# Kernel optimization log

Measured on AMD Instinct MI355X. Metric: run time of the kernel, lower is better.

Reference implementation:

```python
import jax, jax.numpy as jnp
import numpy as np

N = 50000      # nodes
E = 250000     # edges (pairs) per key
DIN = 256
DOUT = 256
OH = 16        # one_hot_length
T = 2          # params['t']


def setup_inputs() -> dict:
    key = jax.random.key(0)
    ks = jax.random.split(key, 16)
    s_in = 1.0 / np.float32(np.sqrt(DIN))
    s_tr = 1.0 / np.float32(np.sqrt(DIN + OH))
    return {
        "h": jax.random.normal(ks[0], (N, DIN), jnp.float32),
        "pairs_k0": jax.random.randint(ks[1], (T, E), 0, N),
        "pairs_k1": jax.random.randint(ks[2], (T, E), 0, N),
        "degrees_k0": jax.random.uniform(ks[3], (T, E, OH), jnp.float32),
        "degrees_k1": jax.random.uniform(ks[4], (T, E, OH), jnp.float32),
        "scatter_k0": jax.random.randint(ks[5], (E,), 0, N),
        "scatter_k1": jax.random.randint(ks[6], (E,), 0, N),
        "W_lin": jax.random.normal(ks[7], (DIN, DOUT), jnp.float32) * s_in,
        "b_lin": jax.random.normal(ks[8], (DOUT,), jnp.float32) * 0.01,
        "W_k0": jax.random.normal(ks[9], (DIN + OH, DOUT), jnp.float32) * s_tr,
        "b_k0": jax.random.normal(ks[10], (DOUT,), jnp.float32) * 0.01,
        "W_k1": jax.random.normal(ks[11], (DIN + OH, DOUT), jnp.float32) * s_tr,
        "b_k1": jax.random.normal(ks[12], (DOUT,), jnp.float32) * 0.01,
        "eps_k0": jnp.zeros((1,), jnp.float32),
        "eps_k1": jnp.zeros((1,), jnp.float32),
    }


def _key_term(h, pairs, degrees, W, b, scatter, eps):
    # combination == 'multi': product over t of sigmoid(Linear([h[pairs_i], deg_i]))
    h_temp = jnp.ones((pairs.shape[1], W.shape[1]), h.dtype)
    for i in range(T):
        h_t = jnp.concatenate([h[pairs[i]], degrees[i]], axis=1)  # [E, DIN+OH]
        h_temp = h_temp * jax.nn.sigmoid(h_t @ W + b)             # [E, DOUT]
    h_sum = jax.ops.segment_sum(h_temp, scatter, num_segments=N)  # [N, DOUT]
    return (1.0 + eps) * h_sum                                    # scalar eps (shape [1])


def reference(h, pairs_k0, pairs_k1, degrees_k0, degrees_k1,
              scatter_k0, scatter_k1, W_lin, b_lin,
              W_k0, b_k0, W_k1, b_k1, eps_k0, eps_k1):
    h3 = h @ W_lin + b_lin
    h3 = h3 + _key_term(h, pairs_k0, degrees_k0, W_k0, b_k0, scatter_k0, eps_k0)
    h3 = h3 + _key_term(h, pairs_k1, degrees_k1, W_k1, b_k1, scatter_k1, eps_k1)
    return h3
```

## Files before the change

kernel.cpp:

```cpp
#include <hip/hip_runtime.h>
#include <hip/hip_bf16.h>

#define N_NODES 50000
#define N_EDGES 250000
#define DIN_ 256
#define DOUT_ 256
#define OH_ 16
#define KF_ 288
#define NBLK_EDGE ((N_EDGES + 63) / 64)
#define NBLK_G ((N_NODES + 63) / 64)
#define SCAN_TOT (2 * N_NODES)
#define SCAN_NB ((SCAN_TOT + 255) / 256)
#define NB_CONV ((N_NODES * DIN_ / 8) / 256)
#define NB_PREP ((DOUT_ * KF_ + 255) / 256)
#define NB_HIST ((N_EDGES + 255) / 256)

typedef short short8 __attribute__((ext_vector_type(8)));
typedef float f32x4 __attribute__((ext_vector_type(4)));

__device__ __forceinline__ unsigned short f2bf(float f) {
    unsigned u = __builtin_bit_cast(unsigned, f);
    return (unsigned short)((u + 0x7fffu + ((u >> 16) & 1u)) >> 16);
}

__device__ __forceinline__ float bf2f(unsigned v) {
    return __builtin_bit_cast(float, v << 16);
}

__device__ __forceinline__ uint4 pack8(float f0, float f1, float f2, float f3,
                                       float f4, float f5, float f6, float f7) {
    uint4 u;
    u.x = (unsigned)f2bf(f0) | ((unsigned)f2bf(f1) << 16);
    u.y = (unsigned)f2bf(f2) | ((unsigned)f2bf(f3) << 16);
    u.z = (unsigned)f2bf(f4) | ((unsigned)f2bf(f5) << 16);
    u.w = (unsigned)f2bf(f6) | ((unsigned)f2bf(f7) << 16);
    return u;
}

__device__ __forceinline__ float fast_rcp(float x) {
#if __has_builtin(__builtin_amdgcn_rcpf)
    return __builtin_amdgcn_rcpf(x);
#else
    return 1.0f / x;
#endif
}

__device__ __forceinline__ void gl_lds16(const void* g, void* l) {
    __builtin_amdgcn_global_load_lds(
        (const __attribute__((address_space(1))) unsigned int*)g,
        (__attribute__((address_space(3))) unsigned int*)l, 16, 0, 0);
}

__global__ void fused_prep(const float* __restrict__ h, unsigned short* __restrict__ hbf,
                           const float* __restrict__ W_lin,
                           const float* __restrict__ W_k0,
                           const float* __restrict__ W_k1,
                           unsigned short* __restrict__ WT_lin,
                           unsigned short* __restrict__ WT_k0,
                           unsigned short* __restrict__ WT_k1,
                           const int* __restrict__ sc0, const int* __restrict__ sc1,
                           int* __restrict__ hist) {
    int bx = blockIdx.x;
    if (bx < NB_CONV) {
        int idx = bx * 256 + threadIdx.x;
        const f32x4* s = (const f32x4*)(h + (size_t)idx * 8);
        f32x4 a = s[0], b = s[1];
        ((uint4*)hbf)[idx] = pack8(a[0], a[1], a[2], a[3], b[0], b[1], b[2], b[3]);
    } else if (bx < NB_CONV + NB_PREP) {
        int idx = (bx - NB_CONV) * 256 + threadIdx.x;
        if (idx < DOUT_ * DIN_) {
            int n = idx >> 8, k = idx & 255;
            WT_lin[idx] = f2bf(W_lin[k * DOUT_ + n]);
        }
        if (idx < DOUT_ * KF_) {
            int n = idx / KF_, k = idx - n * KF_;
            float v0 = 0.f, v1 = 0.f;
            if (k < DIN_ + OH_) {
                v0 = W_k0[k * DOUT_ + n];
                v1 = W_k1[k * DOUT_ + n];
            }
            WT_k0[idx] = f2bf(v0);
            WT_k1[idx] = f2bf(v1);
        }
    } else {
        int e = (bx - NB_CONV - NB_PREP) * 256 + threadIdx.x;
        if (e < N_EDGES) {
            atomicAdd(&hist[sc0[e]], 1);
            atomicAdd(&hist[N_NODES + sc1[e]], 1);
        }
    }
}

__global__ void scan_pass1(const int* __restrict__ hist, int* __restrict__ partials) {
    __shared__ int sdata[256];
    int gid = blockIdx.x * 256 + threadIdx.x;
    sdata[threadIdx.x] = (gid < SCAN_TOT) ? hist[gid] : 0;
    __syncthreads();
    for (int d = 128; d > 0; d >>= 1) {
        if (threadIdx.x < d) sdata[threadIdx.x] += sdata[threadIdx.x + d];
        __syncthreads();
    }
    if (threadIdx.x == 0) partials[blockIdx.x] = sdata[0];
}

__global__ __launch_bounds__(512) void scan_pass2(int* __restrict__ partials) {
    __shared__ int s[512];
    int t = threadIdx.x;
    s[t] = (t < SCAN_NB) ? partials[t] : 0;
    __syncthreads();
    for (int d = 1; d < 512; d <<= 1) {
        int add = (t >= d) ? s[t - d] : 0;
        __syncthreads();
        s[t] += add;
        __syncthreads();
    }
    if (t < SCAN_NB) partials[t] = (t == 0) ? 0 : s[t - 1];
}

__global__ void scan_pass3(const int* __restrict__ hist, const int* __restrict__ partials,
                           int* __restrict__ offs) {
    __shared__ int s[256];
    int gid = blockIdx.x * 256 + threadIdx.x;
    int t = threadIdx.x;
    int v = (gid < SCAN_TOT) ? hist[gid] : 0;
    s[t] = v;
    __syncthreads();
    for (int d = 1; d < 256; d <<= 1) {
        int add = (t >= d) ? s[t - d] : 0;
        __syncthreads();
        s[t] += add;
        __syncthreads();
    }
    if (gid < SCAN_TOT) offs[gid] = partials[blockIdx.x] + s[t] - v;
}

__global__ __launch_bounds__(256) void rank_lin(const int* __restrict__ sc0,
                                                const int* __restrict__ sc1,
                                                int* __restrict__ offs,
                                                int* __restrict__ order,
                                                int* __restrict__ keys,
                                                const unsigned short* __restrict__ hbf,
                                                const unsigned short* __restrict__ WT_lin,
                                                const unsigned short* __restrict__ WTk0,
                                                const unsigned short* __restrict__ WTk1,
                                                const float* __restrict__ b_lin,
                                                const float* __restrict__ bk0,
                                                const float* __restrict__ bk1,
                                                float* __restrict__ out,
                                                unsigned short* __restrict__ G0,
                                                unsigned short* __restrict__ G1) {
    if (blockIdx.x >= 3 * NBLK_G) {
        int e = (blockIdx.x - 3 * NBLK_G) * 256 + threadIdx.x;
        if (e < N_EDGES) {
            int k0 = sc0[e];
            int p = atomicAdd(&offs[k0], 1);
            order[p] = e; keys[p] = k0;
            int k1 = sc1[e];
            int q = atomicAdd(&offs[N_NODES + k1], 1);
            order[q] = e; keys[q] = k1;
        }
        return;
    }
    __shared__ unsigned short Alds[2][64][32];
    __shared__ unsigned short Blds[2][256][32];
    __shared__ float bias_lds[256];
    int kb = blockIdx.x / NBLK_G;
    int bx = blockIdx.x - kb * NBLK_G;
    const unsigned short* WT; const float* bias; int stride;
    if (kb == 0)      { WT = WTk0;   bias = bk0;   stride = KF_; }
    else if (kb == 1) { WT = WTk1;   bias = bk1;   stride = KF_; }
    else              { WT = WT_lin; bias = b_lin; stride = DIN_; }

    int tid = threadIdx.x;
    int w = tid >> 6, ln = tid & 63, l15 = ln & 15;
    int row0 = bx * 64;
    bias_lds[tid] = bias[tid];

    int ar = row0 + w * 16 + (ln >> 2);
    if (ar >= N_NODES) ar = N_NODES - 1;
    int qs = (ln & 3) ^ ((ln >> 3) & 3);
    const unsigned short* asrc = hbf + (size_t)ar * DIN_ + qs * 8;
    int brow = w * 64;
    int swz = ((ln >> 4) ^ ((l15 >> 1) & 3)) * 8;

    f32x4 acc[16];
#pragma unroll
    for (int j = 0; j < 16; ++j) acc[j] = (f32x4)(0.f);

    gl_lds16(asrc, &Alds[0][w * 16][0]);
#pragma unroll
    for (int i = 0; i < 4; ++i) {
        int n = brow + i * 16 + (ln >> 2);
        gl_lds16(WT + (size_t)n * stride + qs * 8, &Blds[0][brow + i * 16][0]);
    }
    __syncthreads();

    int buf = 0;
    for (int kk = 0; kk < 8; ++kk) {
        if (kk < 7) {
            gl_lds16(asrc + (kk + 1) * 32, &Alds[buf ^ 1][w * 16][0]);
#pragma unroll
            for (int i = 0; i < 4; ++i) {
                int n = brow + i * 16 + (ln >> 2);
                gl_lds16(WT + (size_t)n * stride + (kk + 1) * 32 + qs * 8,
                         &Blds[buf ^ 1][brow + i * 16][0]);
            }
        }
        short8 af = *(const short8*)&Alds[buf][w * 16 + l15][swz];
#pragma unroll
        for (int j = 0; j < 16; ++j) {
            short8 bf = *(const short8*)&Blds[buf][j * 16 + l15][swz];
            acc[j] = __builtin_amdgcn_mfma_f32_16x16x32_bf16(af, bf, acc[j], 0, 0, 0);
        }
        __syncthreads();
        buf ^= 1;
    }

    int rbase = row0 + w * 16 + ((ln >> 4) << 2);
    unsigned short* G = (kb == 0) ? G0 : G1;
#pragma unroll
    for (int j = 0; j < 16; ++j) {
        int n = j * 16 + l15;
        float bv = bias_lds[n];
#pragma unroll
        for (int i = 0; i < 4; ++i) {
            int rr = rbase + i;
            if (rr < N_NODES) {
                float v = acc[j][i] + bv;
                if (kb == 2) out[(size_t)rr * DOUT_ + n] = v;
                else         G[(size_t)rr * DOUT_ + n] = f2bf(v);
            }
        }
    }
}

__global__ __launch_bounds__(256, 4) void edge_fused(const unsigned short* __restrict__ Gk0,
                                                     const unsigned short* __restrict__ Gk1,
                                                     const int* __restrict__ pairs0,
                                                     const int* __restrict__ pairs1,
                                                     const float* __restrict__ deg0,
                                                     const float* __restrict__ deg1,
                                                     const int* __restrict__ order_all,
                                                     const int* __restrict__ keys_all,
                                                     const unsigned short* __restrict__ WT0,
                                                     const unsigned short* __restrict__ WT1,
                                                     const float* __restrict__ eps0,
                                                     const float* __restrict__ eps1,
                                                     float* __restrict__ out) {
    __shared__ unsigned int Dlds[4][16][132];
    __shared__ float FL[4][64][2];
    __shared__ int tgt[64], pl0[64], pl1[64], el[64];

    const int nwg = 2 * NBLK_EDGE;
    const int q = nwg / 8, r = nwg % 8;
    int orig = blockIdx.x;
    int xcd = orig & 7;
    int base = orig >> 3;
    int wgid = (xcd < r ? xcd * (q + 1) : r * (q + 1) + (xcd - r) * q) + base;
    int kb = wgid & 1;
    int bx = wgid >> 1;

    const unsigned short* G = kb ? Gk1 : Gk0;
    const int* pairs = kb ? pairs1 : pairs0;
    const float* degrees = kb ? deg1 : deg0;
    const int* order_k = order_all + kb * N_EDGES;
    const int* keys_k  = keys_all + kb * N_EDGES;
    const unsigned short* WT = kb ? WT1 : WT0;
    float epv = 1.0f + (kb ? eps1[0] : eps0[0]);

    int tid = threadIdx.x;
    int w = tid >> 6, ln = tid & 63, l15 = ln & 15, ks = ln >> 4;
    int e0 = bx * 64;
    if (tid < 64) {
        int s = e0 + tid;
        int sc = (s < N_EDGES) ? s : N_EDGES - 1;
        int e = __builtin_nontemporal_load(order_k + sc);
        el[tid]  = e;
        tgt[tid] = (s < N_EDGES) ? __builtin_nontemporal_load(keys_k + s) : -1;
        pl0[tid] = __builtin_nontemporal_load(pairs + e);
        pl1[tid] = __builtin_nontemporal_load(pairs + N_EDGES + e);
    }
    __syncthreads();

    int eA = el[w * 16 + l15];
    f32x4 xa = (f32x4)(0.f), xb = xa, ya = xa, yb = xa;
    if (ks < 2) {
        const f32x4* s0 = (const f32x4*)(degrees + (size_t)eA * OH_ + ks * 8);
        const f32x4* s1 = (const f32x4*)(degrees + ((size_t)N_EDGES + eA) * OH_ + ks * 8);
        xa = __builtin_nontemporal_load(s0);
        xb = __builtin_nontemporal_load(s0 + 1);
        ya = __builtin_nontemporal_load(s1);
        yb = __builtin_nontemporal_load(s1 + 1);
    }

    unsigned int gv[4][16];
#pragma unroll
    for (int r2 = 0; r2 < 16; ++r2) {
        int row = w * 16 + r2;
        const unsigned int* b0 = (const unsigned int*)(G + (size_t)pl0[row] * DOUT_) + ln;
        const unsigned int* b1 = (const unsigned int*)(G + (size_t)pl1[row] * DOUT_) + ln;
        gv[0][r2] = b0[0];
        gv[1][r2] = b1[0];
        gv[2][r2] = b0[64];
        gv[3][r2] = b1[64];
    }
    asm volatile("" ::: "memory");

    short8 a0f = __builtin_bit_cast(short8, pack8(xa[0], xa[1], xa[2], xa[3],
                                                  xb[0], xb[1], xb[2], xb[3]));
    short8 a1f = __builtin_bit_cast(short8, pack8(ya[0], ya[1], ya[2], ya[3],
                                                  yb[0], yb[1], yb[2], yb[3]));
    if (ks >= 2) { a0f = (short8)0; a1f = (short8)0; }

#define MFMA_PHASE(p)                                                                  \
    {                                                                                  \
        f32x4 acc0[8], acc1[8];                                                        \
        _Pragma("unroll")                                                              \
        for (int j = 0; j < 8; ++j) { acc0[j] = (f32x4)(0.f); acc1[j] = (f32x4)(0.f); }\
        _Pragma("unroll")                                                              \
        for (int j = 0; j < 8; ++j) {                                                  \
            int n = (p) * 128 + j * 16 + l15;                                          \
            short8 bf = (short8)0;                                                     \
            if (ks < 2) bf = *(const short8*)(WT + (size_t)n * KF_ + 256 + ks * 8);    \
            acc0[j] = __builtin_amdgcn_mfma_f32_16x16x32_bf16(a0f, bf, acc0[j], 0,0,0);\
            acc1[j] = __builtin_amdgcn_mfma_f32_16x16x32_bf16(a1f, bf, acc1[j], 0,0,0);\
        }                                                                              \
        _Pragma("unroll")                                                              \
        for (int j = 0; j < 8; ++j) {                                                  \
            _Pragma("unroll")                                                          \
            for (int i = 0; i < 4; ++i) {                                              \
                Dlds[w][ks * 4 + i][j * 16 + l15] = (unsigned)f2bf(acc0[j][i])         \
                                                  | ((unsigned)f2bf(acc1[j][i]) << 16);\
            }                                                                          \
        }                                                                              \
    }

#define FLUSH(p, key, r0, r1)                                                          \
    if ((key) >= 0) {                                                                  \
        FL[w][ln][0] = (r0);                                                           \
        FL[w][ln][1] = (r1);                                                           \
        float va = FL[w][(ln >> 1)][ln & 1];                                           \
        float vb = FL[w][32 + (ln >> 1)][ln & 1];                                      \
        atomicAdd(&out[(size_t)(key) * DOUT_ + (p) * 128 + ln], va);                   \
        atomicAdd(&out[(size_t)(key) * DOUT_ + (p) * 128 + 64 + ln], vb);              \
    }

#define REDUCE_PHASE(p, gva, gvb)                                                      \
    {                                                                                  \
        int runkey = tgt[w * 16];                                                      \
        float rs0 = 0.f, rs1 = 0.f;                                                    \
        _Pragma("unroll")                                                              \
        for (int r2 = 0; r2 < 16; ++r2) {                                              \
            int row = w * 16 + r2;                                                     \
            uint2 dp = *(const uint2*)&Dlds[w][r2][2 * ln];                            \
            unsigned int g0u = (gva)[r2], g1u = (gvb)[r2];                             \
            float la0 = bf2f(g0u & 0xffffu) + bf2f(dp.x & 0xffffu);                    \
            float la1 = bf2f(g1u & 0xffffu) + bf2f(dp.x >> 16);                        \
            float ha0 = bf2f(g0u >> 16) + bf2f(dp.y & 0xffffu);                        \
            float ha1 = bf2f(g1u >> 16) + bf2f(dp.y >> 16);                            \
            float v0 = epv * fast_rcp((1.f + __expf(-la0)) * (1.f + __expf(-la1)));    \
            float v1 = epv * fast_rcp((1.f + __expf(-ha0)) * (1.f + __expf(-ha1)));    \
            int k = tgt[row];                                                          \
            if (k != runkey) {                                                         \
                FLUSH(p, runkey, rs0, rs1);                                            \
                runkey = k; rs0 = v0; rs1 = v1;                                        \
            } else { rs0 += v0; rs1 += v1; }                                           \
        }                                                                              \
        FLUSH(p, runkey, rs0, rs1);                                                    \
    }

    MFMA_PHASE(0);
    REDUCE_PHASE(0, gv[0], gv[1]);
    MFMA_PHASE(1);
    REDUCE_PHASE(1, gv[2], gv[3]);

#undef MFMA_PHASE
#undef FLUSH
#undef REDUCE_PHASE
}

extern "C" void kernel_launch(void* const* d_in, const int* in_sizes, int n_in,
                              void* d_out, int out_size, void* d_ws, size_t ws_size,
                              hipStream_t stream) {
    const float* h        = (const float*)d_in[0];
    const int*   pairs_k0 = (const int*)d_in[1];
    const int*   pairs_k1 = (const int*)d_in[2];
    const float* deg_k0   = (const float*)d_in[3];
    const float* deg_k1   = (const float*)d_in[4];
    const int*   sc_k0    = (const int*)d_in[5];
    const int*   sc_k1    = (const int*)d_in[6];
    const float* W_lin    = (const float*)d_in[7];
    const float* b_lin    = (const float*)d_in[8];
    const float* W_k0     = (const float*)d_in[9];
    const float* b_k0     = (const float*)d_in[10];
    const float* W_k1     = (const float*)d_in[11];
    const float* b_k1     = (const float*)d_in[12];
    const float* eps_k0   = (const float*)d_in[13];
    const float* eps_k1   = (const float*)d_in[14];
    float* out = (float*)d_out;

    size_t ush_elems = (size_t)DOUT_ * DIN_ + 2 * (size_t)DOUT_ * KF_
                     + 3 * (size_t)N_NODES * DIN_;
    size_t int_elems = 2 * (size_t)N_NODES * 2 + 2 * (size_t)N_EDGES * 2 + 512;
    size_t need = ush_elems * sizeof(unsigned short) + int_elems * sizeof(int);
    if (ws_size < need) return;

    unsigned short* WT_lin = (unsigned short*)d_ws;
    unsigned short* WT_k0  = WT_lin + DOUT_ * DIN_;
    unsigned short* WT_k1  = WT_k0 + DOUT_ * KF_;
    unsigned short* h_bf   = WT_k1 + DOUT_ * KF_;
    unsigned short* G0     = h_bf + (size_t)N_NODES * DIN_;
    unsigned short* G1     = G0 + (size_t)N_NODES * DIN_;
    int* hist     = (int*)(G1 + (size_t)N_NODES * DIN_);
    int* offs     = hist + 2 * N_NODES;
    int* order    = offs + 2 * N_NODES;
    int* keys     = order + 2 * N_EDGES;
    int* partials = keys + 2 * N_EDGES;

    hipMemsetAsync(hist, 0, 2 * N_NODES * sizeof(int), stream);
    fused_prep<<<NB_CONV + NB_PREP + NB_HIST, 256, 0, stream>>>(
        h, h_bf, W_lin, W_k0, W_k1, WT_lin, WT_k0, WT_k1, sc_k0, sc_k1, hist);
    scan_pass1<<<SCAN_NB, 256, 0, stream>>>(hist, partials);
    scan_pass2<<<1, 512, 0, stream>>>(partials);
    scan_pass3<<<SCAN_NB, 256, 0, stream>>>(hist, partials, offs);
    rank_lin<<<3 * NBLK_G + NB_HIST, 256, 0, stream>>>(
        sc_k0, sc_k1, offs, order, keys, h_bf, WT_lin, WT_k0, WT_k1,
        b_lin, b_k0, b_k1, out, G0, G1);
    edge_fused<<<2 * NBLK_EDGE, 256, 0, stream>>>(G0, G1, pairs_k0, pairs_k1,
                                                  deg_k0, deg_k1, order, keys,
                                                  WT_k0, WT_k1, eps_k0, eps_k1, out);
}
```

Measured before the change: 369.0 us.

## Fold log2e into weights, use exp2 sigmoid, drop LDS flush and XCD remap

Scales the precomputed G projections and the degree-weight rows by log2(e) so the edge kernel can call a native exp2 instead of expf, and folds the sigmoid product into a single fma plus one reciprocal, applying eps only at flush time. The LDS transpose used before the atomic adds is removed, so each lane now atomically adds two adjacent columns directly. The XCD-aware block remapping is replaced by a plain linear split between the two keys. The aim is fewer transcendental and LDS operations per edge, at the cost of less coalesced atomic access patterns and possibly worse L2 locality across XCDs.

```diff
diff --git a/kernel.cpp b/kernel.cpp
--- a/kernel.cpp
+++ b/kernel.cpp
@@ -14,6 +14,7 @@
 #define NB_CONV ((N_NODES * DIN_ / 8) / 256)
 #define NB_PREP ((DOUT_ * KF_ + 255) / 256)
 #define NB_HIST ((N_EDGES + 255) / 256)
+#define LOG2E 1.44269504088896340736f
 
 typedef short short8 __attribute__((ext_vector_type(8)));
 typedef float f32x4 __attribute__((ext_vector_type(4)));
@@ -42,6 +43,14 @@
     return __builtin_amdgcn_rcpf(x);
 #else
     return 1.0f / x;
+#endif
+}
+
+__device__ __forceinline__ float fast_exp2(float x) {
+#if __has_builtin(__builtin_amdgcn_exp2f)
+    return __builtin_amdgcn_exp2f(x);
+#else
+    return exp2f(x);
 #endif
 }
 
@@ -78,6 +87,7 @@
             if (k < DIN_ + OH_) {
                 v0 = W_k0[k * DOUT_ + n];
                 v1 = W_k1[k * DOUT_ + n];
+                if (k >= DIN_) { v0 *= LOG2E; v1 *= LOG2E; }
             }
             WT_k0[idx] = f2bf(v0);
             WT_k1[idx] = f2bf(v1);
@@ -228,7 +238,7 @@
             if (rr < N_NODES) {
                 float v = acc[j][i] + bv;
                 if (kb == 2) out[(size_t)rr * DOUT_ + n] = v;
-                else         G[(size_t)rr * DOUT_ + n] = f2bf(v);
+                else         G[(size_t)rr * DOUT_ + n] = f2bf(v * LOG2E);
             }
         }
     }
@@ -248,18 +258,9 @@
                                                      const float* __restrict__ eps1,
                                                      float* __restrict__ out) {
     __shared__ unsigned int Dlds[4][16][132];
-    __shared__ float FL[4][64][2];
     __shared__ int tgt[64], pl0[64], pl1[64], el[64];
-
-    const int nwg = 2 * NBLK_EDGE;
-    const int q = nwg / 8, r = nwg % 8;
-    int orig = blockIdx.x;
-    int xcd = orig & 7;
-    int base = orig >> 3;
-    int wgid = (xcd < r ? xcd * (q + 1) : r * (q + 1) + (xcd - r) * q) + base;
-    int kb = wgid & 1;
-    int bx = wgid >> 1;
-
+    int kb = (blockIdx.x >= NBLK_EDGE) ? 1 : 0;
+    int bx = blockIdx.x - kb * NBLK_EDGE;
     const unsigned short* G = kb ? Gk1 : Gk0;
     const int* pairs = kb ? pairs1 : pairs0;
     const float* degrees = kb ? deg1 : deg0;
@@ -335,16 +336,6 @@
         }                                                                              \
     }
 
-#define FLUSH(p, key, r0, r1)                                                          \
-    if ((key) >= 0) {                                                                  \
-        FL[w][ln][0] = (r0);                                                           \
-        FL[w][ln][1] = (r1);                                                           \
-        float va = FL[w][(ln >> 1)][ln & 1];                                           \
-        float vb = FL[w][32 + (ln >> 1)][ln & 1];                                      \
-        atomicAdd(&out[(size_t)(key) * DOUT_ + (p) * 128 + ln], va);                   \
-        atomicAdd(&out[(size_t)(key) * DOUT_ + (p) * 128 + 64 + ln], vb);              \
-    }
-
 #define REDUCE_PHASE(p, gva, gvb)                                                      \
     {                                                                                  \
         int runkey = tgt[w * 16];                                                      \
@@ -358,15 +349,27 @@
             float la1 = bf2f(g1u & 0xffffu) + bf2f(dp.x >> 16);                        \
             float ha0 = bf2f(g0u >> 16) + bf2f(dp.y & 0xffffu);                        \
             float ha1 = bf2f(g1u >> 16) + bf2f(dp.y >> 16);                            \
-            float v0 = epv * fast_rcp((1.f + __expf(-la0)) * (1.f + __expf(-la1)));    \
-            float v1 = epv * fast_rcp((1.f + __expf(-ha0)) * (1.f + __expf(-ha1)));    \
+            float ea0 = fast_exp2(-la0), ea1 = fast_exp2(-la1);                        \
+            float eb0 = fast_exp2(-ha0), eb1 = fast_exp2(-ha1);                        \
+            float u0 = 1.f + ea0, u1 = 1.f + eb0;                                      \
+            float v0 = fast_rcp(__builtin_fmaf(u0, ea1, u0));                          \
+            float v1 = fast_rcp(__builtin_fmaf(u1, eb1, u1));                          \
             int k = tgt[row];                                                          \
             if (k != runkey) {                                                         \
-                FLUSH(p, runkey, rs0, rs1);                                            \
+                if (runkey >= 0) {                                                     \
+                    atomicAdd(&out[(size_t)runkey * DOUT_ + (p) * 128 + 2 * ln],       \
+                              epv * rs0);                                              \
+                    atomicAdd(&out[(size_t)runkey * DOUT_ + (p) * 128 + 2 * ln + 1],   \
+                              epv * rs1);                                              \
+                }                                                                      \
                 runkey = k; rs0 = v0; rs1 = v1;                                        \
             } else { rs0 += v0; rs1 += v1; }                                           \
         }                                                                              \
-        FLUSH(p, runkey, rs0, rs1);                                                    \
+        if (runkey >= 0) {                                                             \
+            atomicAdd(&out[(size_t)runkey * DOUT_ + (p) * 128 + 2 * ln], epv * rs0);   \
+            atomicAdd(&out[(size_t)runkey * DOUT_ + (p) * 128 + 2 * ln + 1],           \
+                      epv * rs1);                                                      \
+        }                                                                              \
     }
 
     MFMA_PHASE(0);
@@ -375,7 +378,6 @@
     REDUCE_PHASE(1, gv[2], gv[3]);
 
 #undef MFMA_PHASE
-#undef FLUSH
 #undef REDUCE_PHASE
 }
 
```

After: 424.9 us. 15.1% more time.
